# Kernel tuning notes

Measured on AMD Instinct MI355X. Metric: run time of the kernel, lower is better.

The kernel has to match this reference:

```python
import jax, jax.numpy as jnp
import numpy as np

D_MODEL = 1024
N_HEADS = 16
HEAD_DIM = D_MODEL // N_HEADS  # 64
WINDOW = 64
HALF = WINDOW // 2  # query i attends keys in [i-HALF, i+HALF]
CHUNK = WINDOW      # chunk size for banded attention; must be >= HALF and divide S
B, S = 4, 4096


def setup_inputs() -> dict:
    key = jax.random.key(0)
    ks = jax.random.split(key, 6)
    s = 0.02
    D = D_MODEL
    return {
        "x":  jax.random.normal(ks[0], (B, S, D), jnp.float32),
        "Wq": jax.random.normal(ks[1], (D, D), jnp.float32) * s,
        "bq": jnp.zeros((D,), jnp.float32),
        "Wk": jax.random.normal(ks[2], (D, D), jnp.float32) * s,
        "bk": jnp.zeros((D,), jnp.float32),
        "Wv": jax.random.normal(ks[3], (D, D), jnp.float32) * s,
        "bv": jnp.zeros((D,), jnp.float32),
        "Wo": jax.random.normal(ks[4], (D, D), jnp.float32) * s,
        "bo": jnp.zeros((D,), jnp.float32),
    }


def reference(x, Wq, bq, Wk, bk, Wv, bv, Wo, bo):
    # Sliding-window attention (seq_len > 128 path of SparseAttention).
    b, s, d = x.shape
    h, hd = N_HEADS, HEAD_DIM
    scale = 1.0 / np.sqrt(hd).astype(np.float32)

    q = (x @ Wq.T + bq).reshape(b, s, h, hd)
    k = (x @ Wk.T + bk).reshape(b, s, h, hd)
    v = (x @ Wv.T + bv).reshape(b, s, h, hd)

    c = CHUNK
    nb = s // c
    qc = q.reshape(b, nb, c, h, hd)

    # Pad one chunk of zeros on each side; each query chunk attends keys in
    # chunks [n-1, n, n+1] (covers the +/-HALF band since HALF <= c).
    pad = jnp.zeros((b, c, h, hd), q.dtype)
    kp = jnp.concatenate([pad, k, pad], axis=1).reshape(b, nb + 2, c, h, hd)
    vp = jnp.concatenate([pad, v, pad], axis=1).reshape(b, nb + 2, c, h, hd)
    k3 = jnp.concatenate([kp[:, :-2], kp[:, 1:-1], kp[:, 2:]], axis=2)  # [b,nb,3c,h,hd]
    v3 = jnp.concatenate([vp[:, :-2], vp[:, 1:-1], vp[:, 2:]], axis=2)

    # scores: [b,h,nb,c,3c]
    scores = jnp.einsum('bnqhd,bnkhd->bhnqk', qc, k3) * scale

    # Banded validity mask. Global query pos = n*c + i ; global key pos = n*c + j - c.
    i = jnp.arange(c)[:, None]          # [c,1]
    j = jnp.arange(3 * c)[None, :]      # [1,3c]
    rel = j - c - i                     # key_pos - query_pos, [c,3c]
    band = (rel >= -HALF) & (rel <= HALF)
    n = jnp.arange(nb)[:, None, None]   # [nb,1,1]
    keypos = n * c + (j - c)[None, :, :]  # [nb,1,3c]
    valid = band[None, :, :] & (keypos >= 0) & (keypos < s)  # [nb,c,3c]

    attn = jax.nn.softmax(jnp.where(valid[None, None], scores, -jnp.inf), axis=-1)
    ctx = jnp.einsum('bhnqk,bnkhd->bnqhd', attn, v3).reshape(b, s, d)
    return ctx @ Wo.T + bo
```

## Files before the change

### kernel.cpp

```cpp
#include <hip/hip_runtime.h>
#include <hip/hip_bf16.h>
#include <cstdint>
#include <cstddef>

#define D_MODEL 1024
#define NHEADS  16
#define HDIM    64
#define HALFW   32
#define BATCH   4
#define SEQ     4096
#define MROWS   (BATCH*SEQ)

typedef __attribute__((ext_vector_type(8))) short        bf16x8;
typedef __attribute__((ext_vector_type(4))) float        f32x4;
typedef __attribute__((ext_vector_type(4))) unsigned int u32x4;

typedef const __attribute__((address_space(1))) void gvoid_t;
typedef __attribute__((address_space(3))) void       lvoid_t;

__device__ __forceinline__ unsigned short f2bf(float f) {
    unsigned int u = __float_as_uint(f);
    u += 0x7fffu + ((u >> 16) & 1u);
    return (unsigned short)(u >> 16);
}

__device__ __forceinline__ int vswz(int row, int bytecol) {
    return (row * 256 + bytecol) ^ (((row ^ (row >> 3)) & 7) << 4);
}

__global__ __launch_bounds__(256)
void cvt_f32_bf16(const float* __restrict__ src, unsigned short* __restrict__ dst, int n8) {
    int i = blockIdx.x * 256 + threadIdx.x;
    if (i >= n8) return;
    float4 a = *(const float4*)(src + (size_t)i * 8);
    float4 b = *(const float4*)(src + (size_t)i * 8 + 4);
    u32x4 o;
    o[0] = (unsigned)f2bf(a.x) | ((unsigned)f2bf(a.y) << 16);
    o[1] = (unsigned)f2bf(a.z) | ((unsigned)f2bf(a.w) << 16);
    o[2] = (unsigned)f2bf(b.x) | ((unsigned)f2bf(b.y) << 16);
    o[3] = (unsigned)f2bf(b.z) | ((unsigned)f2bf(b.w) << 16);
    *(u32x4*)(dst + (size_t)i * 8) = o;
}

__global__ __launch_bounds__(256)
void cvt4_f32_bf16(const float* __restrict__ s0, const float* __restrict__ s1,
                   const float* __restrict__ s2, const float* __restrict__ s3,
                   unsigned short* __restrict__ d0, unsigned short* __restrict__ d1,
                   unsigned short* __restrict__ d2, unsigned short* __restrict__ d3, int n8) {
    int i = blockIdx.x * 256 + threadIdx.x;
    if (i >= n8) return;
    const float* src = blockIdx.y == 0 ? s0 : blockIdx.y == 1 ? s1 : blockIdx.y == 2 ? s2 : s3;
    unsigned short* dst = blockIdx.y == 0 ? d0 : blockIdx.y == 1 ? d1 : blockIdx.y == 2 ? d2 : d3;
    float4 a = *(const float4*)(src + (size_t)i * 8);
    float4 b = *(const float4*)(src + (size_t)i * 8 + 4);
    u32x4 o;
    o[0] = (unsigned)f2bf(a.x) | ((unsigned)f2bf(a.y) << 16);
    o[1] = (unsigned)f2bf(a.z) | ((unsigned)f2bf(a.w) << 16);
    o[2] = (unsigned)f2bf(b.x) | ((unsigned)f2bf(b.y) << 16);
    o[3] = (unsigned)f2bf(b.z) | ((unsigned)f2bf(b.w) << 16);
    *(u32x4*)(dst + (size_t)i * 8) = o;
}

template <int CB, int F32OUT>
__global__ __launch_bounds__(256)
void gemm_fused(const unsigned short* __restrict__ A,
                const unsigned short* __restrict__ W0,
                const unsigned short* __restrict__ W1,
                const unsigned short* __restrict__ W2,
                const float* __restrict__ b0, const float* __restrict__ b1,
                const float* __restrict__ b2,
                unsigned short* __restrict__ o0, unsigned short* __restrict__ o1,
                unsigned short* __restrict__ o2, float* __restrict__ of32)
{
    constexpr int K = 1024, N = 1024;
    __shared__ unsigned short As[128 * 32];
    __shared__ unsigned short Bs[128 * 32];
    const int tid  = threadIdx.x;
    const int wave = tid >> 6, lane = tid & 63;
    const int wr = wave >> 1, wc = wave & 1;

    const int bid = blockIdx.x;
    const int x   = bid & 7;
    const int lw  = bid >> 3;
    const int sub = lw / (8 * CB);
    const int l2  = lw % (8 * CB);
    const int cb  = l2 >> 3;
    const int rl  = l2 & 7;
    const int r   = x * 16 + sub * 8 + rl;
    const int which = cb >> 3;
    const int bm = r * 128, bn = (cb & 7) * 128;

    const unsigned short* W = which == 0 ? W0 : (which == 1 ? W1 : W2);
    const float* bias       = which == 0 ? b0 : (which == 1 ? b1 : b2);
    unsigned short* obf     = which == 0 ? o0 : (which == 1 ? o1 : o2);

    f32x4 acc[4][4];
    #pragma unroll
    for (int m = 0; m < 4; ++m)
        #pragma unroll
        for (int n = 0; n < 4; ++n)
            #pragma unroll
            for (int j = 0; j < 4; ++j) acc[m][n][j] = 0.0f;

    const int srow = wave * 32 + (lane >> 2);
    const int scol = (lane & 3) * 8;

    for (int k0 = 0; k0 < K; k0 += 32) {
        #pragma unroll
        for (int rr = 0; rr < 2; ++rr) {
            const int row = srow + rr * 16;
            __builtin_amdgcn_global_load_lds(
                (gvoid_t*)(A + (size_t)(bm + row) * K + k0 + scol),
                (lvoid_t*)(As + (wave * 2 + rr) * 512), 16, 0, 0);
            __builtin_amdgcn_global_load_lds(
                (gvoid_t*)(W + (size_t)(bn + row) * K + k0 + scol),
                (lvoid_t*)(Bs + (wave * 2 + rr) * 512), 16, 0, 0);
        }
        __syncthreads();

        bf16x8 af[4], bw[4];
        #pragma unroll
        for (int m = 0; m < 4; ++m)
            af[m] = *(const bf16x8*)(As + (wr * 64 + m * 16 + (lane & 15)) * 32 + (lane >> 4) * 8);
        #pragma unroll
        for (int n = 0; n < 4; ++n)
            bw[n] = *(const bf16x8*)(Bs + (wc * 64 + n * 16 + (lane & 15)) * 32 + (lane >> 4) * 8);
        #pragma unroll
        for (int m = 0; m < 4; ++m)
            #pragma unroll
            for (int n = 0; n < 4; ++n)
                acc[m][n] = __builtin_amdgcn_mfma_f32_16x16x32_bf16(af[m], bw[n], acc[m][n], 0, 0, 0);
        __syncthreads();
    }

    #pragma unroll
    for (int n = 0; n < 4; ++n) {
        const int col = bn + wc * 64 + n * 16 + (lane & 15);
        const float bv = bias[col];
        #pragma unroll
        for (int m = 0; m < 4; ++m) {
            #pragma unroll
            for (int j = 0; j < 4; ++j) {
                const int row = bm + wr * 64 + m * 16 + (lane >> 4) * 4 + j;
                const float v = acc[m][n][j] + bv;
                if (F32OUT) of32[(size_t)row * N + col] = v;
                else        obf[(size_t)row * N + col]  = f2bf(v);
            }
        }
    }
}

__global__ __launch_bounds__(256)
void attn_band(const unsigned short* __restrict__ Q,
               const unsigned short* __restrict__ Kk,
               const unsigned short* __restrict__ V,
               unsigned short* __restrict__ Ctx)
{
    __shared__ unsigned short Qs[64 * 72];
    __shared__ unsigned short Ks[128 * 72];
    __shared__ unsigned short Vt[64 * 128];
    __shared__ unsigned short Ps[64 * 128];

    const int qt = blockIdx.x, h = blockIdx.y, b = blockIdx.z;
    const int qbase  = qt * 64;
    const int kstart = qbase - HALFW;
    const int tid = threadIdx.x, wave = tid >> 6, lane = tid & 63;

    const size_t base = (size_t)b * SEQ * D_MODEL + (size_t)h * HDIM;
    const unsigned short* Qb = Q  + base;
    const unsigned short* Kb = Kk + base;
    const unsigned short* Vb = V  + base;
    unsigned short*       Cb = Ctx + base;

    for (int c = tid; c < 512; c += 256) {
        const int row = c >> 3, col = (c & 7) * 8;
        *(u32x4*)(Qs + row * 72 + col) =
            *(const u32x4*)(Qb + (size_t)(qbase + row) * D_MODEL + col);
    }
    for (int c = tid; c < 1024; c += 256) {
        const int krow = c >> 3, col = (c & 7) * 8;
        const int kpos = kstart + krow;
        u32x4 kv;
        if (kpos >= 0 && kpos < SEQ) {
            kv = *(const u32x4*)(Kb + (size_t)kpos * D_MODEL + col);
        } else {
            for (int j = 0; j < 4; ++j) kv[j] = 0u;
        }
        *(u32x4*)(Ks + krow * 72 + col) = kv;
    }
    for (int c = tid; c < 512; c += 256) {
        const int p = c >> 3, dch = c & 7;
        const int k0 = kstart + 2 * p, k1 = k0 + 1;
        u32x4 v0, v1;
        if (k0 >= 0 && k0 < SEQ) {
            v0 = *(const u32x4*)(Vb + (size_t)k0 * D_MODEL + dch * 8);
        } else {
            for (int j = 0; j < 4; ++j) v0[j] = 0u;
        }
        if (k1 >= 0 && k1 < SEQ) {
            v1 = *(const u32x4*)(Vb + (size_t)k1 * D_MODEL + dch * 8);
        } else {
            for (int j = 0; j < 4; ++j) v1[j] = 0u;
        }
        #pragma unroll
        for (int j = 0; j < 8; ++j) {
            const int d = dch * 8 + j;
            const unsigned lo = (v0[j >> 1] >> ((j & 1) * 16)) & 0xffffu;
            const unsigned hi = (v1[j >> 1] >> ((j & 1) * 16)) & 0xffffu;
            *(unsigned*)((char*)Vt + vswz(d, 4 * p)) = lo | (hi << 16);
        }
    }
    __syncthreads();

    f32x4 sc[8];
    #pragma unroll
    for (int c = 0; c < 8; ++c)
        #pragma unroll
        for (int j = 0; j < 4; ++j) sc[c][j] = 0.0f;

    bf16x8 aq[2];
    #pragma unroll
    for (int kc = 0; kc < 2; ++kc)
        aq[kc] = *(const bf16x8*)(Qs + (wave * 16 + (lane & 15)) * 72 + kc * 32 + (lane >> 4) * 8);
    #pragma unroll
    for (int c = 0; c < 8; ++c) {
        #pragma unroll
        for (int kc = 0; kc < 2; ++kc) {
            bf16x8 bk_ = *(const bf16x8*)(Ks + (c * 16 + (lane & 15)) * 72 + kc * 32 + (lane >> 4) * 8);
            sc[c] = __builtin_amdgcn_mfma_f32_16x16x32_bf16(aq[kc], bk_, sc[c], 0, 0, 0);
        }
    }

    const int grp = lane >> 4, colk = lane & 15;
    float rowmax[4] = {-1e30f, -1e30f, -1e30f, -1e30f};
    #pragma unroll
    for (int c = 0; c < 8; ++c) {
        const int kpos = kstart + c * 16 + colk;
        #pragma unroll
        for (int j = 0; j < 4; ++j) {
            const int qpos = qbase + wave * 16 + grp * 4 + j;
            const int rel = kpos - qpos;
            const bool valid = (kpos >= 0) && (kpos < SEQ) && (rel >= -HALFW) && (rel <= HALFW);
            const float v = valid ? sc[c][j] * 0.125f : -1e30f;
            sc[c][j] = v;
            rowmax[j] = fmaxf(rowmax[j], v);
        }
    }
    #pragma unroll
    for (int j = 0; j < 4; ++j)
        #pragma unroll
        for (int m = 1; m < 16; m <<= 1)
            rowmax[j] = fmaxf(rowmax[j], __shfl_xor(rowmax[j], m, 64));

    float rowsum[4] = {0.f, 0.f, 0.f, 0.f};
    #pragma unroll
    for (int c = 0; c < 8; ++c)
        #pragma unroll
        for (int j = 0; j < 4; ++j) {
            const float p = __expf(sc[c][j] - rowmax[j]);
            sc[c][j] = p;
            rowsum[j] += p;
        }
    #pragma unroll
    for (int j = 0; j < 4; ++j)
        #pragma unroll
        for (int m = 1; m < 16; m <<= 1)
            rowsum[j] += __shfl_xor(rowsum[j], m, 64);

    #pragma unroll
    for (int c = 0; c < 8; ++c)
        #pragma unroll
        for (int j = 0; j < 4; ++j)
            *(unsigned short*)((char*)Ps + vswz(wave * 16 + grp * 4 + j, (c * 16 + colk) * 2))
                = f2bf(sc[c][j]);
    __syncthreads();

    f32x4 o[4];
    #pragma unroll
    for (int n = 0; n < 4; ++n)
        #pragma unroll
        for (int j = 0; j < 4; ++j) o[n][j] = 0.0f;
    #pragma unroll
    for (int kc = 0; kc < 4; ++kc) {
        bf16x8 pa = *(const bf16x8*)((const char*)Ps +
                        vswz(wave * 16 + (lane & 15), kc * 64 + (lane >> 4) * 16));
        #pragma unroll
        for (int n = 0; n < 4; ++n) {
            bf16x8 bv_ = *(const bf16x8*)((const char*)Vt +
                            vswz(n * 16 + (lane & 15), kc * 64 + (lane >> 4) * 16));
            o[n] = __builtin_amdgcn_mfma_f32_16x16x32_bf16(pa, bv_, o[n], 0, 0, 0);
        }
    }

    float rinv[4];
    #pragma unroll
    for (int j = 0; j < 4; ++j) rinv[j] = 1.0f / rowsum[j];
    #pragma unroll
    for (int n = 0; n < 4; ++n)
        #pragma unroll
        for (int j = 0; j < 4; ++j) {
            const int q = qbase + wave * 16 + grp * 4 + j;
            Cb[(size_t)q * D_MODEL + n * 16 + colk] = f2bf(o[n][j] * rinv[j]);
        }
}

extern "C" void kernel_launch(void* const* d_in, const int* in_sizes, int n_in,
                              void* d_out, int out_size, void* d_ws, size_t ws_size,
                              hipStream_t stream)
{
    (void)in_sizes; (void)n_in; (void)out_size; (void)ws_size;
    const float* x  = (const float*)d_in[0];
    const float* Wq = (const float*)d_in[1];
    const float* bq = (const float*)d_in[2];
    const float* Wk = (const float*)d_in[3];
    const float* bk = (const float*)d_in[4];
    const float* Wv = (const float*)d_in[5];
    const float* bv = (const float*)d_in[6];
    const float* Wo = (const float*)d_in[7];
    const float* bo = (const float*)d_in[8];
    float* out = (float*)d_out;

    char* ws = (char*)d_ws;
    unsigned short* xb  = (unsigned short*)ws;
    unsigned short* wqb = (unsigned short*)(ws + 33554432);
    unsigned short* wkb = wqb + 1048576;
    unsigned short* wvb = wkb + 1048576;
    unsigned short* wob = wvb + 1048576;
    unsigned short* qb  = wob + 1048576;
    unsigned short* kb  = qb + (size_t)MROWS * D_MODEL;
    unsigned short* vb  = kb + (size_t)MROWS * D_MODEL;
    unsigned short* ctxb = xb;

    cvt_f32_bf16<<<dim3(MROWS * D_MODEL / 8 / 256), 256, 0, stream>>>(x, xb, MROWS * D_MODEL / 8);
    cvt4_f32_bf16<<<dim3(D_MODEL * D_MODEL / 8 / 256, 4), 256, 0, stream>>>(
        Wq, Wk, Wv, Wo, wqb, wkb, wvb, wob, D_MODEL * D_MODEL / 8);

    gemm_fused<24, 0><<<dim3(128 * 24), 256, 0, stream>>>(
        xb, wqb, wkb, wvb, bq, bk, bv, qb, kb, vb, nullptr);

    attn_band<<<dim3(SEQ / 64, NHEADS, BATCH), 256, 0, stream>>>(qb, kb, vb, ctxb);

    gemm_fused<8, 1><<<dim3(128 * 8), 256, 0, stream>>>(
        ctxb, wob, wob, wob, bo, bo, bo, nullptr, nullptr, nullptr, out);
}
```

Measured before the change: 256.0 us.

## Replace GEMM with 256x256-tile, 4-stage pipelined, swizzled-LDS MFMA kernel

```diff
diff --git a/kernel.cpp b/kernel.cpp
--- a/kernel.cpp
+++ b/kernel.cpp
@@ -61,90 +61,129 @@
     *(u32x4*)(dst + (size_t)i * 8) = o;
 }
 
-template <int CB, int F32OUT>
-__global__ __launch_bounds__(256)
-void gemm_fused(const unsigned short* __restrict__ A,
-                const unsigned short* __restrict__ W0,
-                const unsigned short* __restrict__ W1,
-                const unsigned short* __restrict__ W2,
-                const float* __restrict__ b0, const float* __restrict__ b1,
-                const float* __restrict__ b2,
-                unsigned short* __restrict__ o0, unsigned short* __restrict__ o1,
-                unsigned short* __restrict__ o2, float* __restrict__ of32)
+template <int NOUT, int F32OUT>
+__global__ __launch_bounds__(512)
+void gemm256(const unsigned short* __restrict__ A,
+             const unsigned short* __restrict__ W0,
+             const unsigned short* __restrict__ W1,
+             const unsigned short* __restrict__ W2,
+             const float* __restrict__ b0, const float* __restrict__ b1,
+             const float* __restrict__ b2,
+             unsigned short* __restrict__ o0, unsigned short* __restrict__ o1,
+             unsigned short* __restrict__ o2, float* __restrict__ of32)
 {
-    constexpr int K = 1024, N = 1024;
-    __shared__ unsigned short As[128 * 32];
-    __shared__ unsigned short Bs[128 * 32];
+    constexpr int K  = 1024;
+    constexpr int NT = K / 32;
+    constexpr int NWG = 64 * 4 * NOUT;
+    __shared__ unsigned short lds[65536];
+
     const int tid  = threadIdx.x;
     const int wave = tid >> 6, lane = tid & 63;
-    const int wr = wave >> 1, wc = wave & 1;
+    const int wr = wave >> 2, wc = wave & 3;
 
     const int bid = blockIdx.x;
-    const int x   = bid & 7;
-    const int lw  = bid >> 3;
-    const int sub = lw / (8 * CB);
-    const int l2  = lw % (8 * CB);
-    const int cb  = l2 >> 3;
-    const int rl  = l2 & 7;
-    const int r   = x * 16 + sub * 8 + rl;
-    const int which = cb >> 3;
-    const int bm = r * 128, bn = (cb & 7) * 128;
-
-    const unsigned short* W = which == 0 ? W0 : (which == 1 ? W1 : W2);
-    const float* bias       = which == 0 ? b0 : (which == 1 ? b1 : b2);
-    unsigned short* obf     = which == 0 ? o0 : (which == 1 ? o1 : o2);
-
-    f32x4 acc[4][4];
-    #pragma unroll
-    for (int m = 0; m < 4; ++m)
+    const int g   = (bid & 7) * (NWG / 8) + (bid >> 3);
+    const int rb  = g / (4 * NOUT);
+    const int cb  = g % (4 * NOUT);
+    const int which = cb >> 2;
+    const int bm = rb * 256, bn = (cb & 3) * 256;
+
+    const unsigned short* W = (NOUT == 1 || which == 0) ? W0 : (which == 1 ? W1 : W2);
+    const float* bias       = (NOUT == 1 || which == 0) ? b0 : (which == 1 ? b1 : b2);
+    unsigned short* obf     = (NOUT == 1 || which == 0) ? o0 : (which == 1 ? o1 : o2);
+
+    f32x4 acc[8][4];
+    #pragma unroll
+    for (int m = 0; m < 8; ++m)
         #pragma unroll
         for (int n = 0; n < 4; ++n)
             #pragma unroll
             for (int j = 0; j < 4; ++j) acc[m][n][j] = 0.0f;
 
-    const int srow = wave * 32 + (lane >> 2);
-    const int scol = (lane & 3) * 8;
-
-    for (int k0 = 0; k0 < K; k0 += 32) {
-        #pragma unroll
-        for (int rr = 0; rr < 2; ++rr) {
-            const int row = srow + rr * 16;
-            __builtin_amdgcn_global_load_lds(
-                (gvoid_t*)(A + (size_t)(bm + row) * K + k0 + scol),
-                (lvoid_t*)(As + (wave * 2 + rr) * 512), 16, 0, 0);
-            __builtin_amdgcn_global_load_lds(
-                (gvoid_t*)(W + (size_t)(bn + row) * K + k0 + scol),
-                (lvoid_t*)(Bs + (wave * 2 + rr) * 512), 16, 0, 0);
-        }
-        __syncthreads();
-
-        bf16x8 af[4], bw[4];
+    const int r0  = tid >> 2;
+    const int ks0 = (tid & 3) ^ (r0 & 3);
+    const size_t aoff0 = (size_t)(bm + r0)       * K + ks0 * 8;
+    const size_t aoff1 = (size_t)(bm + r0 + 128) * K + ks0 * 8;
+    const size_t boff0 = (size_t)(bn + r0)       * K + ks0 * 8;
+    const size_t boff1 = (size_t)(bn + r0 + 128) * K + ks0 * 8;
+    const int stW = wave * 1024;
+
+    char* ldsb = (char*)lds;
+
+    auto STAGE_A = [&](int t) {
+        const int slot = (t & 3) * 32768;
+        const int kt = t * 32;
+        __builtin_amdgcn_global_load_lds((gvoid_t*)(A + aoff0 + kt),
+            (lvoid_t*)(ldsb + slot + stW), 16, 0, 0);
+        __builtin_amdgcn_global_load_lds((gvoid_t*)(A + aoff1 + kt),
+            (lvoid_t*)(ldsb + slot + 8192 + stW), 16, 0, 0);
+    };
+    auto STAGE_B = [&](int t) {
+        const int slot = (t & 3) * 32768 + 16384;
+        const int kt = t * 32;
+        __builtin_amdgcn_global_load_lds((gvoid_t*)(W + boff0 + kt),
+            (lvoid_t*)(ldsb + slot + stW), 16, 0, 0);
+        __builtin_amdgcn_global_load_lds((gvoid_t*)(W + boff1 + kt),
+            (lvoid_t*)(ldsb + slot + 8192 + stW), 16, 0, 0);
+    };
+
+    const int lr  = lane & 15;
+    const int xb_ = ((lane >> 4) ^ (lane & 3)) << 4;
+    const int aread = (wr * 128 + lr) * 64 + xb_;
+    const int bread = 16384 + (wc * 64 + lr) * 64 + xb_;
+
+    STAGE_A(0); STAGE_B(0); STAGE_A(1); STAGE_B(1); STAGE_A(2); STAGE_B(2);
+    asm volatile("s_waitcnt vmcnt(8)" ::: "memory");
+    __builtin_amdgcn_s_barrier();
+
+    for (int t = 0; t < NT; ++t) {
+        const char* sl = ldsb + (t & 3) * 32768;
+        bf16x8 a_lo[4], bfr[4];
         #pragma unroll
         for (int m = 0; m < 4; ++m)
-            af[m] = *(const bf16x8*)(As + (wr * 64 + m * 16 + (lane & 15)) * 32 + (lane >> 4) * 8);
+            a_lo[m] = *(const bf16x8*)(sl + aread + m * 1024);
         #pragma unroll
         for (int n = 0; n < 4; ++n)
-            bw[n] = *(const bf16x8*)(Bs + (wc * 64 + n * 16 + (lane & 15)) * 32 + (lane >> 4) * 8);
+            bfr[n] = *(const bf16x8*)(sl + bread + n * 1024);
+        if (t + 3 < NT) STAGE_A(t + 3);
+        __builtin_amdgcn_s_barrier();
+        __builtin_amdgcn_s_setprio(1);
         #pragma unroll
         for (int m = 0; m < 4; ++m)
             #pragma unroll
             for (int n = 0; n < 4; ++n)
-                acc[m][n] = __builtin_amdgcn_mfma_f32_16x16x32_bf16(af[m], bw[n], acc[m][n], 0, 0, 0);
-        __syncthreads();
+                acc[m][n] = __builtin_amdgcn_mfma_f32_16x16x32_bf16(a_lo[m], bfr[n], acc[m][n], 0, 0, 0);
+        __builtin_amdgcn_s_setprio(0);
+        __builtin_amdgcn_s_barrier();
+        bf16x8 a_hi[4];
+        #pragma unroll
+        for (int m = 0; m < 4; ++m)
+            a_hi[m] = *(const bf16x8*)(sl + aread + 4096 + m * 1024);
+        if (t + 3 < NT) STAGE_B(t + 3);
+        asm volatile("s_waitcnt vmcnt(8)" ::: "memory");
+        __builtin_amdgcn_s_barrier();
+        __builtin_amdgcn_s_setprio(1);
+        #pragma unroll
+        for (int m = 0; m < 4; ++m)
+            #pragma unroll
+            for (int n = 0; n < 4; ++n)
+                acc[m + 4][n] = __builtin_amdgcn_mfma_f32_16x16x32_bf16(a_hi[m], bfr[n], acc[m + 4][n], 0, 0, 0);
+        __builtin_amdgcn_s_setprio(0);
+        __builtin_amdgcn_s_barrier();
     }
 
     #pragma unroll
     for (int n = 0; n < 4; ++n) {
-        const int col = bn + wc * 64 + n * 16 + (lane & 15);
+        const int col = bn + wc * 64 + n * 16 + lr;
         const float bv = bias[col];
         #pragma unroll
-        for (int m = 0; m < 4; ++m) {
+        for (int m = 0; m < 8; ++m) {
             #pragma unroll
             for (int j = 0; j < 4; ++j) {
-                const int row = bm + wr * 64 + m * 16 + (lane >> 4) * 4 + j;
+                const int row = bm + wr * 128 + m * 16 + (lane >> 4) * 4 + j;
                 const float v = acc[m][n][j] + bv;
-                if (F32OUT) of32[(size_t)row * N + col] = v;
-                else        obf[(size_t)row * N + col]  = f2bf(v);
+                if (F32OUT) of32[(size_t)row * 1024 + col] = v;
+                else        obf[(size_t)row * 1024 + col]  = f2bf(v);
             }
         }
     }
@@ -335,11 +374,11 @@
     cvt4_f32_bf16<<<dim3(D_MODEL * D_MODEL / 8 / 256, 4), 256, 0, stream>>>(
         Wq, Wk, Wv, Wo, wqb, wkb, wvb, wob, D_MODEL * D_MODEL / 8);
 
-    gemm_fused<24, 0><<<dim3(128 * 24), 256, 0, stream>>>(
+    gemm256<3, 0><<<dim3(768), 512, 0, stream>>>(
         xb, wqb, wkb, wvb, bq, bk, bv, qb, kb, vb, nullptr);
 
     attn_band<<<dim3(SEQ / 64, NHEADS, BATCH), 256, 0, stream>>>(qb, kb, vb, ctxb);
 
-    gemm_fused<8, 1><<<dim3(128 * 8), 256, 0, stream>>>(
+    gemm256<1, 1><<<dim3(256), 512, 0, stream>>>(
         ctxb, wob, wob, wob, bo, bo, bo, nullptr, nullptr, nullptr, out);
 }
```

Result: faster. 245.3 us (-4.2%).
